# Kernel tuning notes

Hardware: AMD Instinct MI355X
Metric: run time of the kernel (lower is better)

The kernel has to match this reference:

```python
import math
import jax, jax.numpy as jnp
import numpy as np

B, L, DIM, H = 2, 2048, 1024, 16
HD = DIM // H  # 64
EPS = 1e-6


def _rms_norm(x):
    # x: [..., d] float32; no learned weight (trainable=False)
    norm = jax.lax.rsqrt(jnp.mean(jnp.square(x), axis=-1, keepdims=True) + EPS)
    return x * norm


def _apply_rotary(x, cos, sin):
    # x: [b, h, l, d]; cos/sin: [1, 1, l, d//2]
    d = x.shape[-1] // 2
    x1, x2 = x[..., :d], x[..., d:]
    y1 = x1 * cos + x2 * sin
    y2 = -x1 * sin + x2 * cos
    return jnp.concatenate([y1, y2], axis=-1)


def setup_inputs() -> dict:
    key = jax.random.key(0)
    ks = jax.random.split(key, 6)
    s = 0.02
    return {
        "x": jax.random.normal(ks[0], (B, L, DIM), dtype=jnp.float32),
        "v_0": jax.random.normal(ks[1], (B, H, L, HD), dtype=jnp.float32),
        "rope_cos": jnp.cos(jax.random.normal(ks[2], (1, 1, L, HD // 2), dtype=jnp.float32)),
        "rope_sin": jnp.sin(jax.random.normal(ks[2], (1, 1, L, HD // 2), dtype=jnp.float32)),
        "qkv_w": jax.random.normal(ks[3], (3 * DIM, DIM), dtype=jnp.float32) * s,
        "proj_w": jax.random.normal(ks[4], (DIM, DIM), dtype=jnp.float32) * s,
        "lambda_param": jnp.full((1,), 0.5, dtype=jnp.float32),
    }


def reference(x, v_0, rope_cos, rope_sin, qkv_w, proj_w, lambda_param):
    b, l, dim = x.shape
    # QKV projection (no bias): [b, l, 3*dim]
    qkv = jnp.einsum('bld,ed->ble', x, qkv_w)
    # rearrange 'b l (k h d) -> k b h l d'
    qkv = qkv.reshape(b, l, 3, H, HD).transpose(2, 0, 3, 1, 4)
    q, k, v = qkv[0], qkv[1], qkv[2]
    # residual-v blend
    lam = lambda_param.reshape(())
    v = lam * v + (1.0 - lam) * v_0
    # RoPE (done in float32, inputs already float32)
    q = _apply_rotary(q, rope_cos, rope_sin)
    k = _apply_rotary(k, rope_cos, rope_sin)
    # dynamic softmax temperature
    ratio = math.sqrt(math.log(l) / math.log(1040.0))
    k = k * ratio
    # QKNorm (RMSNorm over head_dim, no weight)
    q = _rms_norm(q)
    k = _rms_norm(k)
    # scaled dot product attention
    scale = 1.0 / math.sqrt(HD)
    scores = jnp.einsum('bhqd,bhkd->bhqk', q, k) * scale
    attn = jax.nn.softmax(scores, axis=-1)
    out = jnp.einsum('bhqk,bhkd->bhqd', attn, v)
    # 'b h l d -> b l (h d)' then output projection (no bias)
    out = out.transpose(0, 2, 1, 3).reshape(b, l, dim)
    out = jnp.einsum('bld,ed->ble', out, proj_w)
    return (out, v)
```

## Files before the change

kernel.cpp:

```cpp
#include <hip/hip_runtime.h>

typedef _Float16 f16;
typedef _Float16 f16x8 __attribute__((ext_vector_type(8)));
typedef _Float16 f16x4 __attribute__((ext_vector_type(4)));
typedef float f32x4 __attribute__((ext_vector_type(4)));

#define MFMA32(a, b, c) __builtin_amdgcn_mfma_f32_16x16x32_f16((a), (b), (c), 0, 0, 0)

constexpr int Bs = 2, Ls = 2048, DIM = 1024, NH = 16, HD = 64;
constexpr int BL = Bs * Ls;
constexpr float EPSV = 1e-6f;
constexpr float SCL2 = 0.125f * 1.44269504f;

__device__ __forceinline__ void async16(void* lds, const void* g) {
  __builtin_amdgcn_global_load_lds((const __attribute__((address_space(1))) void*)g,
                                   (__attribute__((address_space(3))) void*)lds, 16, 0, 0);
}

__device__ __forceinline__ int sw32(int r, int q) {
  int p = r >> 1;
  return p * 64 + ((((r & 1) * 4 + q) ^ (p & 7)) * 8);
}

__global__ void cvt_all_kernel(const float* __restrict__ x, const float* __restrict__ wq,
                               const float* __restrict__ wp, f16* __restrict__ xf,
                               f16* __restrict__ wqf, f16* __restrict__ wpf) {
  constexpr int NX4 = BL * DIM / 4;
  constexpr int NW4 = 3 * DIM * DIM / 4;
  int i = blockIdx.x * blockDim.x + threadIdx.x;
  const float4* src;
  f16x4* dst;
  int j;
  if (i < NX4) {
    src = (const float4*)x; dst = (f16x4*)xf; j = i;
  } else if (i < NX4 + NW4) {
    src = (const float4*)wq; dst = (f16x4*)wqf; j = i - NX4;
  } else {
    src = (const float4*)wp; dst = (f16x4*)wpf; j = i - NX4 - NW4;
  }
  float4 a = src[j];
  f16x4 o = {(f16)a.x, (f16)a.y, (f16)a.z, (f16)a.w};
  dst[j] = o;
}

__global__ __launch_bounds__(256) void qkv_gemm_kernel(
    const f16* __restrict__ A, const f16* __restrict__ W,
    const float* __restrict__ v0,
    const float* __restrict__ rcos, const float* __restrict__ rsin,
    const float* __restrict__ lamp,
    f16* __restrict__ qb, f16* __restrict__ kb, f16* __restrict__ vbT,
    float* __restrict__ vout) {
  constexpr int K = DIM;
  __shared__ alignas(16) f16 sA[128 * 32];
  __shared__ alignas(16) f16 sB[128 * 32];
  const int tid = threadIdx.x;
  const int w = tid >> 6, lane = tid & 63, ln = lane & 15, quad = lane >> 4;
  const int wm = w >> 1, wn = w & 1;
  const int m0 = blockIdx.y * 128, n0 = blockIdx.x * 128;

  const f16* gA[2];
  const f16* gB[2];
#pragma unroll
  for (int s = 0; s < 2; ++s) {
    int lc = tid + s * 256;
    int p = lc >> 3, g = (lc & 7) ^ (p & 7);
    int r = 2 * p + (g >> 2), ce = (g & 3) * 8;
    gA[s] = A + (size_t)(m0 + r) * K + ce;
    gB[s] = W + (size_t)(n0 + r) * K + ce;
  }

  f32x4 acc[4][4] = {};

  for (int it = 0; it < 32; ++it) {
    const int k0 = it * 32;
#pragma unroll
    for (int s = 0; s < 2; ++s) {
      async16(&sA[(tid + s * 256) * 8], gA[s] + k0);
      async16(&sB[(tid + s * 256) * 8], gB[s] + k0);
    }
    __syncthreads();
    f16x8 a[4];
#pragma unroll
    for (int mi = 0; mi < 4; ++mi)
      a[mi] = *(const f16x8*)&sA[sw32(wm * 64 + mi * 16 + ln, quad)];
#pragma unroll
    for (int ni = 0; ni < 4; ++ni) {
      f16x8 b = *(const f16x8*)&sB[sw32(wn * 64 + ni * 16 + ln, quad)];
#pragma unroll
      for (int mi = 0; mi < 4; ++mi) acc[mi][ni] = MFMA32(a[mi], b, acc[mi][ni]);
    }
    __syncthreads();
  }

  const int nb = n0 + wn * 64;
  const int nsec = nb >> 10;
  const int h = (nb & 1023) >> 6;

  if (nsec == 2) {
    const float lam = lamp[0];
#pragma unroll
    for (int mi = 0; mi < 4; ++mi) {
#pragma unroll
      for (int rg = 0; rg < 4; ++rg) {
        int row = m0 + wm * 64 + mi * 16 + quad * 4 + rg;
        int b = row >> 11, l = row & 2047;
        size_t base = ((size_t)(b * NH + h) * Ls + l) * HD;
        int key = l & 63;
        int sidx = ((key >> 2) & 3) * 16 + (key >> 4) * 4 + (key & 3);
        size_t tb = ((size_t)(b * NH + h) * HD) * Ls + (l & ~63) + sidx;
#pragma unroll
        for (int ni = 0; ni < 4; ++ni) {
          int d = ni * 16 + ln;
          float vnew = lam * acc[mi][ni][rg] + (1.0f - lam) * v0[base + d];
          vout[base + d] = vnew;
          vbT[tb + (size_t)d * Ls] = (f16)vnew;
        }
      }
    }
  } else {
    f16* dst = nsec ? kb : qb;
    const float ratio = sqrtf(logf(2048.0f) / logf(1040.0f));
    const float post = nsec ? 1.0f : SCL2;
#pragma unroll
    for (int mi = 0; mi < 4; ++mi) {
#pragma unroll
      for (int rg = 0; rg < 4; ++rg) {
        int row = m0 + wm * 64 + mi * 16 + quad * 4 + rg;
        int b = row >> 11, l = row & 2047;
        float vals[4];
#pragma unroll
        for (int ni = 0; ni < 4; ++ni) vals[ni] = acc[mi][ni][rg];
#pragma unroll
        for (int t = 0; t < 2; ++t) {
          int j = t * 16 + ln;
          float c = rcos[l * 32 + j], s = rsin[l * 32 + j];
          float x1 = vals[t], x2 = vals[t + 2];
          vals[t] = x1 * c + x2 * s;
          vals[t + 2] = -x1 * s + x2 * c;
        }
        if (nsec) {
#pragma unroll
          for (int ni = 0; ni < 4; ++ni) vals[ni] *= ratio;
        }
        float ms = vals[0] * vals[0] + vals[1] * vals[1] + vals[2] * vals[2] + vals[3] * vals[3];
        ms += __shfl_xor(ms, 1);
        ms += __shfl_xor(ms, 2);
        ms += __shfl_xor(ms, 4);
        ms += __shfl_xor(ms, 8);
        float rn = rsqrtf(ms * (1.0f / 64.0f) + EPSV) * post;
        size_t base = ((size_t)(b * NH + h) * Ls + l) * HD;
#pragma unroll
        for (int ni = 0; ni < 4; ++ni) dst[base + ni * 16 + ln] = (f16)(vals[ni] * rn);
      }
    }
  }
}

__global__ __launch_bounds__(512, 4) void flash_kernel(
    const f16* __restrict__ qg, const f16* __restrict__ kg, const f16* __restrict__ vtg,
    f16* __restrict__ ao) {
  __shared__ alignas(16) f16 sK[2][2][64 * 64];
  __shared__ alignas(16) f16 sVT[2][2][64 * 64];
  const int tid = threadIdx.x;
  const int w = tid >> 6, lane = tid & 63, ln = lane & 15, quad = lane >> 4;
  const int grp = w >> 2, wl = w & 3;
  const int gt = tid & 255;
  const int bx = blockIdx.x;
  const int bh = bx & 31, qt = bx >> 5;
  const int h = bh & 15, b = bh >> 4;
  const f16* Qh = qg + (size_t)(b * NH + h) * Ls * HD;
  const f16* Kh = kg + (size_t)(b * NH + h) * Ls * HD;
  const f16* VTh = vtg + (size_t)(b * NH + h) * HD * Ls;
  const int q0 = qt * 128;

  f16x8 aq[2][2];
#pragma unroll
  for (int st = 0; st < 2; ++st)
#pragma unroll
    for (int kk = 0; kk < 2; ++kk)
      aq[st][kk] = *(const f16x8*)&Qh[(size_t)(q0 + wl * 32 + st * 16 + ln) * HD + kk * 32 + quad * 8];

  f16x8 kr[2], vr[2];
  auto loadKV = [&](int k0) {
#pragma unroll
    for (int s = 0; s < 2; ++s) {
      int ch = gt + s * 256, r = ch >> 3, cg = (ch & 7) * 8;
      kr[s] = *(const f16x8*)&Kh[(size_t)(k0 + r) * HD + cg];
      vr[s] = *(const f16x8*)&VTh[(size_t)r * Ls + k0 + cg];
    }
  };
  auto stageKV = [&](int buf) {
#pragma unroll
    for (int s = 0; s < 2; ++s) {
      int ch = gt + s * 256, r = ch >> 3;
      int po = r * 64 + (((ch & 7) ^ (r & 7)) * 8);
      *(f16x8*)&sK[grp][buf][po] = kr[s];
      *(f16x8*)&sVT[grp][buf][po] = vr[s];
    }
  };

  f32x4 O[2][4] = {};
  f32x4 racc[2] = {};
  const f16x8 onesv = {(f16)1.f, (f16)1.f, (f16)1.f, (f16)1.f,
                       (f16)1.f, (f16)1.f, (f16)1.f, (f16)1.f};
  const f32x4 zc = {};

  const int kbase = grp << 10;
  loadKV(kbase);
  stageKV(0);
  __syncthreads();

  for (int t = 0; t < 16; ++t) {
    const int cur = t & 1;
    if (t < 15) loadKV(kbase + (t + 1) * 64);

    f16x8 pA[2][2];
#pragma unroll
    for (int nt = 0; nt < 4; ++nt) {
      const int r = nt * 16 + ln;
      const f16x8 kf0 = *(const f16x8*)&sK[grp][cur][r * 64 + ((quad ^ (r & 7)) * 8)];
      const f16x8 kf1 = *(const f16x8*)&sK[grp][cur][r * 64 + (((4 + quad) ^ (r & 7)) * 8)];
#pragma unroll
      for (int st = 0; st < 2; ++st) {
        f32x4 z = MFMA32(kf1, aq[st][1], MFMA32(kf0, aq[st][0], zc));
#pragma unroll
        for (int j = 0; j < 4; ++j)
          pA[st][nt >> 1][(nt & 1) * 4 + j] = (f16)exp2f(z[j]);
      }
    }

    __builtin_amdgcn_s_setprio(1);
#pragma unroll
    for (int st = 0; st < 2; ++st) {
      racc[st] = MFMA32(pA[st][0], onesv, racc[st]);
      racc[st] = MFMA32(pA[st][1], onesv, racc[st]);
    }
#pragma unroll
    for (int dt = 0; dt < 4; ++dt) {
      const int row = dt * 16 + ln;
#pragma unroll
      for (int nt2 = 0; nt2 < 2; ++nt2) {
        const f16x8 vf = *(const f16x8*)&sVT[grp][cur][row * 64 + (((quad * 2 + nt2) ^ (row & 7)) * 8)];
#pragma unroll
        for (int st = 0; st < 2; ++st)
          O[st][dt] = MFMA32(pA[st][nt2], vf, O[st][dt]);
      }
    }
    __builtin_amdgcn_s_setprio(0);

    if (t < 15) stageKV(cur ^ 1);
    __syncthreads();
  }

  float* cO = (float*)&sK[0][0][0];
  float* cR = (float*)&sVT[0][0][0];
  if (grp == 1) {
#pragma unroll
    for (int st = 0; st < 2; ++st) {
#pragma unroll
      for (int rg = 0; rg < 4; ++rg) {
        const int ql = wl * 32 + st * 16 + quad * 4 + rg;
#pragma unroll
        for (int dt = 0; dt < 4; ++dt) cO[ql * 64 + dt * 16 + ln] = O[st][dt][rg];
        if (ln == 0) cR[ql] = racc[st][rg];
      }
    }
  }
  __syncthreads();
  if (grp == 0) {
#pragma unroll
    for (int st = 0; st < 2; ++st) {
#pragma unroll
      for (int rg = 0; rg < 4; ++rg) {
        const int ql = wl * 32 + st * 16 + quad * 4 + rg;
        const float inv = 1.0f / (racc[st][rg] + cR[ql]);
        const int q = q0 + ql;
        const size_t orow = ((size_t)b * Ls + q) * DIM + h * HD;
#pragma unroll
        for (int dt = 0; dt < 4; ++dt)
          ao[orow + dt * 16 + ln] = (f16)((O[st][dt][rg] + cO[ql * 64 + dt * 16 + ln]) * inv);
      }
    }
  }
}

__global__ __launch_bounds__(256) void proj_gemm_kernel(
    const f16* __restrict__ A, const f16* __restrict__ W, float* __restrict__ out) {
  constexpr int K = DIM;
  __shared__ alignas(16) f16 sA[64 * 32];
  __shared__ alignas(16) f16 sB[128 * 32];
  const int tid = threadIdx.x;
  const int w = tid >> 6, lane = tid & 63, ln = lane & 15, quad = lane >> 4;
  const int wm = w >> 1, wn = w & 1;
  const int m0 = blockIdx.y * 64, n0 = blockIdx.x * 128;

  const f16* gA;
  {
    int p = tid >> 3, g = (tid & 7) ^ (p & 7);
    gA = A + (size_t)(m0 + 2 * p + (g >> 2)) * K + (g & 3) * 8;
  }
  const f16* gB[2];
#pragma unroll
  for (int s = 0; s < 2; ++s) {
    int lc = tid + s * 256;
    int p = lc >> 3, g = (lc & 7) ^ (p & 7);
    gB[s] = W + (size_t)(n0 + 2 * p + (g >> 2)) * K + (g & 3) * 8;
  }

  f32x4 acc[2][4] = {};

  for (int it = 0; it < 32; ++it) {
    const int k0 = it * 32;
    async16(&sA[tid * 8], gA + k0);
#pragma unroll
    for (int s = 0; s < 2; ++s) async16(&sB[(tid + s * 256) * 8], gB[s] + k0);
    __syncthreads();
    f16x8 a[2];
#pragma unroll
    for (int mi = 0; mi < 2; ++mi)
      a[mi] = *(const f16x8*)&sA[sw32(wm * 32 + mi * 16 + ln, quad)];
#pragma unroll
    for (int ni = 0; ni < 4; ++ni) {
      f16x8 b = *(const f16x8*)&sB[sw32(wn * 64 + ni * 16 + ln, quad)];
#pragma unroll
      for (int mi = 0; mi < 2; ++mi) acc[mi][ni] = MFMA32(a[mi], b, acc[mi][ni]);
    }
    __syncthreads();
  }

#pragma unroll
  for (int mi = 0; mi < 2; ++mi) {
#pragma unroll
    for (int rg = 0; rg < 4; ++rg) {
      int row = m0 + wm * 32 + mi * 16 + quad * 4 + rg;
      size_t o = (size_t)row * DIM + n0 + wn * 64;
#pragma unroll
      for (int ni = 0; ni < 4; ++ni) out[o + ni * 16 + ln] = acc[mi][ni][rg];
    }
  }
}

extern "C" void kernel_launch(void* const* d_in, const int* in_sizes, int n_in,
                              void* d_out, int out_size, void* d_ws, size_t ws_size,
                              hipStream_t stream) {
  (void)in_sizes; (void)n_in; (void)out_size; (void)ws_size;
  const float* x = (const float*)d_in[0];
  const float* v0 = (const float*)d_in[1];
  const float* rcos = (const float*)d_in[2];
  const float* rsin = (const float*)d_in[3];
  const float* wqkv = (const float*)d_in[4];
  const float* wproj = (const float*)d_in[5];
  const float* lamp = (const float*)d_in[6];
  float* out = (float*)d_out;
  float* vout = out + (size_t)BL * DIM;

  char* p = (char*)d_ws;
  auto take = [&](size_t n) { char* q = p; p += ((n + 255) / 256) * 256; return q; };
  f16* xf = (f16*)take((size_t)BL * DIM * 2);
  f16* wqf = (f16*)take((size_t)3 * DIM * DIM * 2);
  f16* wpf = (f16*)take((size_t)DIM * DIM * 2);
  f16* qb = (f16*)take((size_t)BL * DIM * 2);
  f16* kb = (f16*)take((size_t)BL * DIM * 2);
  f16* vbT = (f16*)take((size_t)BL * DIM * 2);
  f16* ao = xf;

  constexpr int NCVT4 = (BL * DIM + 3 * DIM * DIM + DIM * DIM) / 4;
  cvt_all_kernel<<<dim3(NCVT4 / 256), dim3(256), 0, stream>>>(x, wqkv, wproj, xf, wqf, wpf);

  qkv_gemm_kernel<<<dim3(3 * DIM / 128, BL / 128), dim3(256), 0, stream>>>(
      xf, wqf, v0, rcos, rsin, lamp, qb, kb, vbT, vout);

  flash_kernel<<<dim3(Bs * NH * (Ls / 128)), dim3(512), 0, stream>>>(qb, kb, vbT, ao);

  proj_gemm_kernel<<<dim3(DIM / 128, BL / 64), dim3(256), 0, stream>>>(ao, wpf, out);
}
```

Baseline: 224.2 us.

## Fuse x fp16 conversion into QKV GEMM with double-buffered pipelining

Drops the separate conversion of x to fp16. The QKV GEMM now loads fp32 x into registers, converts it and writes it to LDS, which removes one full read-and-write pass over the activations. The K loop becomes double-buffered so the next tile's loads overlap with the current MFMAs, and blocks are remapped to a 1D grid with a swizzle for better L2 locality. The V-transpose epilogue is staged through LDS to give coalesced vector stores, at the cost of more LDS use and more register pressure from the in-flight fp32 loads.

```diff
diff --git a/kernel.cpp b/kernel.cpp
--- a/kernel.cpp
+++ b/kernel.cpp
@@ -22,21 +22,17 @@
   return p * 64 + ((((r & 1) * 4 + q) ^ (p & 7)) * 8);
 }
 
-__global__ void cvt_all_kernel(const float* __restrict__ x, const float* __restrict__ wq,
-                               const float* __restrict__ wp, f16* __restrict__ xf,
-                               f16* __restrict__ wqf, f16* __restrict__ wpf) {
-  constexpr int NX4 = BL * DIM / 4;
+__global__ void cvt_w_kernel(const float* __restrict__ wq, const float* __restrict__ wp,
+                             f16* __restrict__ wqf, f16* __restrict__ wpf) {
   constexpr int NW4 = 3 * DIM * DIM / 4;
   int i = blockIdx.x * blockDim.x + threadIdx.x;
   const float4* src;
   f16x4* dst;
   int j;
-  if (i < NX4) {
-    src = (const float4*)x; dst = (f16x4*)xf; j = i;
-  } else if (i < NX4 + NW4) {
-    src = (const float4*)wq; dst = (f16x4*)wqf; j = i - NX4;
+  if (i < NW4) {
+    src = (const float4*)wq; dst = (f16x4*)wqf; j = i;
   } else {
-    src = (const float4*)wp; dst = (f16x4*)wpf; j = i - NX4 - NW4;
+    src = (const float4*)wp; dst = (f16x4*)wpf; j = i - NW4;
   }
   float4 a = src[j];
   f16x4 o = {(f16)a.x, (f16)a.y, (f16)a.z, (f16)a.w};
@@ -44,51 +40,78 @@
 }
 
 __global__ __launch_bounds__(256) void qkv_gemm_kernel(
-    const f16* __restrict__ A, const f16* __restrict__ W,
+    const float* __restrict__ X, const f16* __restrict__ W,
     const float* __restrict__ v0,
     const float* __restrict__ rcos, const float* __restrict__ rsin,
     const float* __restrict__ lamp,
     f16* __restrict__ qb, f16* __restrict__ kb, f16* __restrict__ vbT,
     float* __restrict__ vout) {
   constexpr int K = DIM;
-  __shared__ alignas(16) f16 sA[128 * 32];
-  __shared__ alignas(16) f16 sB[128 * 32];
+  __shared__ alignas(16) f16 sm[4][128 * 32];
   const int tid = threadIdx.x;
   const int w = tid >> 6, lane = tid & 63, ln = lane & 15, quad = lane >> 4;
   const int wm = w >> 1, wn = w & 1;
-  const int m0 = blockIdx.y * 128, n0 = blockIdx.x * 128;
-
-  const f16* gA[2];
+
+  const int wg = ((blockIdx.x & 7) * 96) + (blockIdx.x >> 3);
+  const int m0 = (wg / 24) * 128, n0 = (wg % 24) * 128;
+
+  const float* gAx[2];
   const f16* gB[2];
 #pragma unroll
   for (int s = 0; s < 2; ++s) {
     int lc = tid + s * 256;
     int p = lc >> 3, g = (lc & 7) ^ (p & 7);
     int r = 2 * p + (g >> 2), ce = (g & 3) * 8;
-    gA[s] = A + (size_t)(m0 + r) * K + ce;
+    gAx[s] = X + (size_t)(m0 + r) * K + ce;
     gB[s] = W + (size_t)(n0 + r) * K + ce;
   }
 
+  float4 ar[2][2];
+  auto loadA = [&](int k0) {
+#pragma unroll
+    for (int s = 0; s < 2; ++s) {
+      const float* pa = gAx[s] + k0;
+      ar[s][0] = *(const float4*)pa;
+      ar[s][1] = *(const float4*)(pa + 4);
+    }
+  };
+  auto writeA = [&](int buf) {
+#pragma unroll
+    for (int s = 0; s < 2; ++s) {
+      f16x8 h8 = {(f16)ar[s][0].x, (f16)ar[s][0].y, (f16)ar[s][0].z, (f16)ar[s][0].w,
+                  (f16)ar[s][1].x, (f16)ar[s][1].y, (f16)ar[s][1].z, (f16)ar[s][1].w};
+      *(f16x8*)&sm[buf][(tid + s * 256) * 8] = h8;
+    }
+  };
+  auto issueB = [&](int k0, int buf) {
+#pragma unroll
+    for (int s = 0; s < 2; ++s) async16(&sm[2 + buf][(tid + s * 256) * 8], gB[s] + k0);
+  };
+
   f32x4 acc[4][4] = {};
 
+  loadA(0);
+  issueB(0, 0);
+  writeA(0);
+  __syncthreads();
+
   for (int it = 0; it < 32; ++it) {
-    const int k0 = it * 32;
-#pragma unroll
-    for (int s = 0; s < 2; ++s) {
-      async16(&sA[(tid + s * 256) * 8], gA[s] + k0);
-      async16(&sB[(tid + s * 256) * 8], gB[s] + k0);
-    }
-    __syncthreads();
+    const int cur = it & 1, nxt = cur ^ 1;
+    if (it < 31) {
+      loadA((it + 1) * 32);
+      issueB((it + 1) * 32, nxt);
+    }
     f16x8 a[4];
 #pragma unroll
     for (int mi = 0; mi < 4; ++mi)
-      a[mi] = *(const f16x8*)&sA[sw32(wm * 64 + mi * 16 + ln, quad)];
+      a[mi] = *(const f16x8*)&sm[cur][sw32(wm * 64 + mi * 16 + ln, quad)];
 #pragma unroll
     for (int ni = 0; ni < 4; ++ni) {
-      f16x8 b = *(const f16x8*)&sB[sw32(wn * 64 + ni * 16 + ln, quad)];
+      f16x8 b = *(const f16x8*)&sm[2 + cur][sw32(wn * 64 + ni * 16 + ln, quad)];
 #pragma unroll
       for (int mi = 0; mi < 4; ++mi) acc[mi][ni] = MFMA32(a[mi], b, acc[mi][ni]);
     }
+    if (it < 31) writeA(nxt);
     __syncthreads();
   }
 
@@ -98,24 +121,37 @@
 
   if (nsec == 2) {
     const float lam = lamp[0];
+    const int l064 = m0 + wm * 64;
+    const int b = l064 >> 11, l0 = l064 & 2047;
+    const size_t vb = (size_t)(b * NH + h) * Ls * HD;
+    f16* wT = &sm[0][0] + w * 4096;
+    __syncthreads();
 #pragma unroll
     for (int mi = 0; mi < 4; ++mi) {
 #pragma unroll
-      for (int rg = 0; rg < 4; ++rg) {
-        int row = m0 + wm * 64 + mi * 16 + quad * 4 + rg;
-        int b = row >> 11, l = row & 2047;
-        size_t base = ((size_t)(b * NH + h) * Ls + l) * HD;
-        int key = l & 63;
-        int sidx = ((key >> 2) & 3) * 16 + (key >> 4) * 4 + (key & 3);
-        size_t tb = ((size_t)(b * NH + h) * HD) * Ls + (l & ~63) + sidx;
-#pragma unroll
-        for (int ni = 0; ni < 4; ++ni) {
-          int d = ni * 16 + ln;
-          float vnew = lam * acc[mi][ni][rg] + (1.0f - lam) * v0[base + d];
-          vout[base + d] = vnew;
-          vbT[tb + (size_t)d * Ls] = (f16)vnew;
+      for (int ni = 0; ni < 4; ++ni) {
+        const int d = ni * 16 + ln;
+        f16 pk[4];
+#pragma unroll
+        for (int rg = 0; rg < 4; ++rg) {
+          const int kk = mi * 16 + quad * 4 + rg;
+          const size_t base = vb + (size_t)(l0 + kk) * HD + d;
+          float vnew = lam * acc[mi][ni][rg] + (1.0f - lam) * v0[base];
+          vout[base] = vnew;
+          pk[rg] = (f16)vnew;
         }
-      }
+        f16x4 q4 = {pk[0], pk[1], pk[2], pk[3]};
+        const int sidx0 = quad * 16 + mi * 4;
+        *(f16x4*)&wT[d * 64 + (sidx0 ^ ((d & 7) << 3))] = q4;
+      }
+    }
+    __syncthreads();
+    const size_t tB = (size_t)(b * NH + h) * HD * Ls + l0;
+#pragma unroll
+    for (int dd = 0; dd < 16; ++dd) {
+      const int d = dd * 4 + quad;
+      f16x4 vv = *(const f16x4*)&wT[d * 64 + ((ln * 4) ^ ((d & 7) << 3))];
+      *(f16x4*)&vbT[tB + (size_t)d * Ls + ln * 4] = vv;
     }
   } else {
     f16* dst = nsec ? kb : qb;
@@ -356,19 +392,18 @@
 
   char* p = (char*)d_ws;
   auto take = [&](size_t n) { char* q = p; p += ((n + 255) / 256) * 256; return q; };
-  f16* xf = (f16*)take((size_t)BL * DIM * 2);
+  f16* ao = (f16*)take((size_t)BL * DIM * 2);
   f16* wqf = (f16*)take((size_t)3 * DIM * DIM * 2);
   f16* wpf = (f16*)take((size_t)DIM * DIM * 2);
   f16* qb = (f16*)take((size_t)BL * DIM * 2);
   f16* kb = (f16*)take((size_t)BL * DIM * 2);
   f16* vbT = (f16*)take((size_t)BL * DIM * 2);
-  f16* ao = xf;
-
-  constexpr int NCVT4 = (BL * DIM + 3 * DIM * DIM + DIM * DIM) / 4;
-  cvt_all_kernel<<<dim3(NCVT4 / 256), dim3(256), 0, stream>>>(x, wqkv, wproj, xf, wqf, wpf);
-
-  qkv_gemm_kernel<<<dim3(3 * DIM / 128, BL / 128), dim3(256), 0, stream>>>(
-      xf, wqf, v0, rcos, rsin, lamp, qb, kb, vbT, vout);
+
+  constexpr int NCVT4 = (3 * DIM * DIM + DIM * DIM) / 4;
+  cvt_w_kernel<<<dim3(NCVT4 / 256), dim3(256), 0, stream>>>(wqkv, wproj, wqf, wpf);
+
+  qkv_gemm_kernel<<<dim3(3 * DIM / 128 * (BL / 128)), dim3(256), 0, stream>>>(
+      x, wqf, v0, rcos, rsin, lamp, qb, kb, vbT, vout);
 
   flash_kernel<<<dim3(Bs * NH * (Ls / 128)), dim3(512), 0, stream>>>(qb, kb, vbT, ao);
 
```

Result: slower. 243.5 us (+8.6%).

## Double-buffer GEMM LDS loads, remap QKV blocks per XCD, stage V transpose in LDS

Applied to the files above, without the earlier changes.

Both the QKV and projection GEMMs now double-buffer their LDS tiles, so the next K-slice's async global-to-LDS loads are issued before the MFMAs on the current slice run. This is meant to hide load latency behind compute. The QKV grid is flattened and the block index remapped so consecutive tiles land on the same XCD (groups of 96), aiming for better L2 reuse. The transposed V write now goes through a swizzled LDS buffer, so global stores are vectorized instead of scattered 2-byte writes. The cost is twice the LDS footprint, which may lower occupancy.

```diff
diff --git a/kernel.cpp b/kernel.cpp
--- a/kernel.cpp
+++ b/kernel.cpp
@@ -51,12 +51,13 @@
     f16* __restrict__ qb, f16* __restrict__ kb, f16* __restrict__ vbT,
     float* __restrict__ vout) {
   constexpr int K = DIM;
-  __shared__ alignas(16) f16 sA[128 * 32];
-  __shared__ alignas(16) f16 sB[128 * 32];
+  __shared__ alignas(16) f16 sm[4][128 * 32];
   const int tid = threadIdx.x;
   const int w = tid >> 6, lane = tid & 63, ln = lane & 15, quad = lane >> 4;
   const int wm = w >> 1, wn = w & 1;
-  const int m0 = blockIdx.y * 128, n0 = blockIdx.x * 128;
+
+  const int wg = ((blockIdx.x & 7) * 96) + (blockIdx.x >> 3);
+  const int m0 = (wg / 24) * 128, n0 = (wg % 24) * 128;
 
   const f16* gA[2];
   const f16* gB[2];
@@ -69,23 +70,29 @@
     gB[s] = W + (size_t)(n0 + r) * K + ce;
   }
 
+  auto issue = [&](int k0, int buf) {
+#pragma unroll
+    for (int s = 0; s < 2; ++s) {
+      async16(&sm[buf][(tid + s * 256) * 8], gA[s] + k0);
+      async16(&sm[2 + buf][(tid + s * 256) * 8], gB[s] + k0);
+    }
+  };
+
   f32x4 acc[4][4] = {};
 
+  issue(0, 0);
+  __syncthreads();
+
   for (int it = 0; it < 32; ++it) {
-    const int k0 = it * 32;
-#pragma unroll
-    for (int s = 0; s < 2; ++s) {
-      async16(&sA[(tid + s * 256) * 8], gA[s] + k0);
-      async16(&sB[(tid + s * 256) * 8], gB[s] + k0);
-    }
-    __syncthreads();
+    const int cur = it & 1;
+    if (it < 31) issue((it + 1) * 32, cur ^ 1);
     f16x8 a[4];
 #pragma unroll
     for (int mi = 0; mi < 4; ++mi)
-      a[mi] = *(const f16x8*)&sA[sw32(wm * 64 + mi * 16 + ln, quad)];
+      a[mi] = *(const f16x8*)&sm[cur][sw32(wm * 64 + mi * 16 + ln, quad)];
 #pragma unroll
     for (int ni = 0; ni < 4; ++ni) {
-      f16x8 b = *(const f16x8*)&sB[sw32(wn * 64 + ni * 16 + ln, quad)];
+      f16x8 b = *(const f16x8*)&sm[2 + cur][sw32(wn * 64 + ni * 16 + ln, quad)];
 #pragma unroll
       for (int mi = 0; mi < 4; ++mi) acc[mi][ni] = MFMA32(a[mi], b, acc[mi][ni]);
     }
@@ -98,24 +105,35 @@
 
   if (nsec == 2) {
     const float lam = lamp[0];
+    const int l064 = m0 + wm * 64;
+    const int b = l064 >> 11, l0 = l064 & 2047;
+    const size_t vb = (size_t)(b * NH + h) * Ls * HD;
+    f16* wT = &sm[0][0] + w * 4096;
 #pragma unroll
     for (int mi = 0; mi < 4; ++mi) {
 #pragma unroll
-      for (int rg = 0; rg < 4; ++rg) {
-        int row = m0 + wm * 64 + mi * 16 + quad * 4 + rg;
-        int b = row >> 11, l = row & 2047;
-        size_t base = ((size_t)(b * NH + h) * Ls + l) * HD;
-        int key = l & 63;
-        int sidx = ((key >> 2) & 3) * 16 + (key >> 4) * 4 + (key & 3);
-        size_t tb = ((size_t)(b * NH + h) * HD) * Ls + (l & ~63) + sidx;
-#pragma unroll
-        for (int ni = 0; ni < 4; ++ni) {
-          int d = ni * 16 + ln;
-          float vnew = lam * acc[mi][ni][rg] + (1.0f - lam) * v0[base + d];
-          vout[base + d] = vnew;
-          vbT[tb + (size_t)d * Ls] = (f16)vnew;
+      for (int ni = 0; ni < 4; ++ni) {
+        const int d = ni * 16 + ln;
+        f16 pk[4];
+#pragma unroll
+        for (int rg = 0; rg < 4; ++rg) {
+          const int kk = mi * 16 + quad * 4 + rg;
+          const size_t base = vb + (size_t)(l0 + kk) * HD + d;
+          float vnew = lam * acc[mi][ni][rg] + (1.0f - lam) * v0[base];
+          vout[base] = vnew;
+          pk[rg] = (f16)vnew;
         }
-      }
+        f16x4 q4 = {pk[0], pk[1], pk[2], pk[3]};
+        const int sidx0 = quad * 16 + mi * 4;
+        *(f16x4*)&wT[d * 64 + (sidx0 ^ ((d & 7) << 3))] = q4;
+      }
+    }
+    const size_t tB = (size_t)(b * NH + h) * HD * Ls + l0;
+#pragma unroll
+    for (int dd = 0; dd < 16; ++dd) {
+      const int d = dd * 4 + quad;
+      f16x4 vv = *(const f16x4*)&wT[d * 64 + ((ln * 4) ^ ((d & 7) << 3))];
+      *(f16x4*)&vbT[tB + (size_t)d * Ls + ln * 4] = vv;
     }
   } else {
     f16* dst = nsec ? kb : qb;
@@ -287,8 +305,8 @@
 __global__ __launch_bounds__(256) void proj_gemm_kernel(
     const f16* __restrict__ A, const f16* __restrict__ W, float* __restrict__ out) {
   constexpr int K = DIM;
-  __shared__ alignas(16) f16 sA[64 * 32];
-  __shared__ alignas(16) f16 sB[128 * 32];
+  __shared__ alignas(16) f16 sA[2][64 * 32];
+  __shared__ alignas(16) f16 sB[2][128 * 32];
   const int tid = threadIdx.x;
   const int w = tid >> 6, lane = tid & 63, ln = lane & 15, quad = lane >> 4;
   const int wm = w >> 1, wn = w & 1;
@@ -307,21 +325,27 @@
     gB[s] = W + (size_t)(n0 + 2 * p + (g >> 2)) * K + (g & 3) * 8;
   }
 
+  auto issue = [&](int k0, int buf) {
+    async16(&sA[buf][tid * 8], gA + k0);
+#pragma unroll
+    for (int s = 0; s < 2; ++s) async16(&sB[buf][(tid + s * 256) * 8], gB[s] + k0);
+  };
+
   f32x4 acc[2][4] = {};
 
+  issue(0, 0);
+  __syncthreads();
+
   for (int it = 0; it < 32; ++it) {
-    const int k0 = it * 32;
-    async16(&sA[tid * 8], gA + k0);
-#pragma unroll
-    for (int s = 0; s < 2; ++s) async16(&sB[(tid + s * 256) * 8], gB[s] + k0);
-    __syncthreads();
+    const int cur = it & 1;
+    if (it < 31) issue((it + 1) * 32, cur ^ 1);
     f16x8 a[2];
 #pragma unroll
     for (int mi = 0; mi < 2; ++mi)
-      a[mi] = *(const f16x8*)&sA[sw32(wm * 32 + mi * 16 + ln, quad)];
+      a[mi] = *(const f16x8*)&sA[cur][sw32(wm * 32 + mi * 16 + ln, quad)];
 #pragma unroll
     for (int ni = 0; ni < 4; ++ni) {
-      f16x8 b = *(const f16x8*)&sB[sw32(wn * 64 + ni * 16 + ln, quad)];
+      f16x8 b = *(const f16x8*)&sB[cur][sw32(wn * 64 + ni * 16 + ln, quad)];
 #pragma unroll
       for (int mi = 0; mi < 2; ++mi) acc[mi][ni] = MFMA32(a[mi], b, acc[mi][ni]);
     }
@@ -367,7 +391,7 @@
   constexpr int NCVT4 = (BL * DIM + 3 * DIM * DIM + DIM * DIM) / 4;
   cvt_all_kernel<<<dim3(NCVT4 / 256), dim3(256), 0, stream>>>(x, wqkv, wproj, xf, wqf, wpf);
 
-  qkv_gemm_kernel<<<dim3(3 * DIM / 128, BL / 128), dim3(256), 0, stream>>>(
+  qkv_gemm_kernel<<<dim3(3 * DIM / 128 * (BL / 128)), dim3(256), 0, stream>>>(
       xf, wqf, v0, rcos, rsin, lamp, qb, kb, vbT, vout);
 
   flash_kernel<<<dim3(Bs * NH * (Ls / 128)), dim3(512), 0, stream>>>(qb, kb, vbT, ao);
```

Measured after the change: 231.6 us. 1.03x slower.
